# Optimization experiments

Hardware: AMD Instinct MI355X
Metric: run time of the kernel (lower is better)

Reference implementation:

```python
import jax, jax.numpy as jnp
import numpy as np

USER_NUM = 100000
ITEM_NUM = 50000
N_NODES = USER_NUM + ITEM_NUM
EMB_DIM = 64
N_LAYERS = 3
NNZ = 4800000


def setup_inputs() -> dict:
    key = jax.random.key(0)
    k1, k2, k3, k4, k5 = jax.random.split(key, 5)
    user_emb = 0.2 * jax.random.normal(k1, (USER_NUM, EMB_DIM), dtype=jnp.float32)
    item_emb = 0.2 * jax.random.normal(k2, (ITEM_NUM, EMB_DIM), dtype=jnp.float32)
    adj_row = jax.random.randint(k3, (NNZ,), 0, N_NODES, dtype=jnp.int32)
    adj_col = jax.random.randint(k4, (NNZ,), 0, N_NODES, dtype=jnp.int32)
    adj_vals = jax.random.uniform(k5, (NNZ,), dtype=jnp.float32)
    return {
        "user_emb": user_emb,
        "item_emb": item_emb,
        "adj_row": adj_row,
        "adj_col": adj_col,
        "adj_vals": adj_vals,
    }


def _spmm(row, col, vals, x):
    # sparse [N,N] @ dense [N,D] via gather + weighted segment-sum
    msg = vals[:, None] * x[col]  # [nnz, D]
    return jax.ops.segment_sum(msg, row, num_segments=N_NODES)


def reference(user_emb, item_emb, adj_row, adj_col, adj_vals):
    ego = jnp.concatenate([user_emb, item_emb], axis=0)  # [N, D]
    acc = ego  # running sum over layers (equivalent to stack+mean)
    for _ in range(N_LAYERS):
        ego = _spmm(adj_row, adj_col, adj_vals, ego)
        acc = acc + ego
    out = acc / jnp.asarray(N_LAYERS + 1, dtype=acc.dtype)
    return out[:USER_NUM], out[USER_NUM:]
```

## Files before the change

kernel.cpp:

```cpp
#include <hip/hip_runtime.h>

#define USER_NUM 100000
#define ITEM_NUM 50000
#define N_NODES  150000
#define EMB_DIM  64
#define NNZ      4800000

#define CB_SHIFT 10
#define ROWS_PER_CB 1024
#define NCB ((N_NODES + ROWS_PER_CB - 1) / ROWS_PER_CB)
#define CB_CAP 34000
#define TILE 8192
#define NTILES ((NNZ + TILE - 1) / TILE)
#define EPT 32

__device__ __forceinline__ float bflo(unsigned u) {
    return __uint_as_float(u << 16);
}
__device__ __forceinline__ float bfhi(unsigned u) {
    return __uint_as_float(u & 0xFFFF0000u);
}
__device__ __forceinline__ unsigned f2bf(float f) {
    unsigned u = __float_as_uint(f);
    return (u + 0x7FFFu + ((u >> 16) & 1u)) >> 16;
}

__global__ void lgcn_init(const float4* __restrict__ user,
                          const float4* __restrict__ item,
                          uint4* __restrict__ xb,
                          float4* __restrict__ acc) {
    int i = blockIdx.x * blockDim.x + threadIdx.x;
    if (i >= N_NODES * 8) return;
    const int user_chunks = USER_NUM * 8;
    float4 f0, f1;
    if (i < user_chunks) {
        f0 = user[i * 2];
        f1 = user[i * 2 + 1];
    } else {
        f0 = item[(i - user_chunks) * 2];
        f1 = item[(i - user_chunks) * 2 + 1];
    }
    acc[i * 2]     = f0;
    acc[i * 2 + 1] = f1;
    uint4 p;
    p.x = f2bf(f0.x) | (f2bf(f0.y) << 16);
    p.y = f2bf(f0.z) | (f2bf(f0.w) << 16);
    p.z = f2bf(f1.x) | (f2bf(f1.y) << 16);
    p.w = f2bf(f1.z) | (f2bf(f1.w) << 16);
    xb[i] = p;
}

__global__ void lgcn_bcur_init(int* __restrict__ bucket_cursor) {
    int b = blockIdx.x * blockDim.x + threadIdx.x;
    if (b < NCB) bucket_cursor[b] = b * CB_CAP;
}

__global__ __launch_bounds__(256) void lgcn_partition(
    const int* __restrict__ row,
    const int* __restrict__ col,
    const float* __restrict__ vals,
    int* __restrict__ bucket_cursor,
    int2* __restrict__ t_cv) {
    __shared__ int hist[NCB];
    __shared__ int excl[NCB];
    __shared__ int delta[NCB];
    __shared__ unsigned lslot[TILE];
    __shared__ int sscan[256];

    int tid = threadIdx.x;
    int tileStart = blockIdx.x * TILE;
    int tileCount = NNZ - tileStart;
    if (tileCount > TILE) tileCount = TILE;

    for (int b = tid; b < NCB; b += 256) hist[b] = 0;
    __syncthreads();

    int rws[EPT];
#pragma unroll
    for (int k = 0; k < EPT; ++k) {
        int le = tid + k * 256;
        int r = -1;
        if (le < tileCount) {
            r = row[tileStart + le];
            atomicAdd(&hist[r >> CB_SHIFT], 1);
        }
        rws[k] = r;
    }
    __syncthreads();

    int h = (tid < NCB) ? hist[tid] : 0;
    sscan[tid] = h;
    __syncthreads();
    for (int off = 1; off < 256; off <<= 1) {
        int x = (tid >= off) ? sscan[tid - off] : 0;
        __syncthreads();
        sscan[tid] += x;
        __syncthreads();
    }
    if (tid < NCB) {
        int ex = sscan[tid] - h;
        excl[tid] = ex;
        int rb = h ? atomicAdd(&bucket_cursor[tid], h) : 0;
        delta[tid] = rb - ex;
    }
    __syncthreads();

#pragma unroll
    for (int k = 0; k < EPT; ++k) {
        int le = tid + k * 256;
        if (le < tileCount) {
            int r = rws[k];
            int b = r >> CB_SHIFT;
            int lp = atomicAdd(&excl[b], 1);
            lslot[lp] = ((unsigned)b << 23) |
                        ((unsigned)(r & (ROWS_PER_CB - 1)) << 13) |
                        (unsigned)le;
        }
    }
    __syncthreads();

    for (int i = tid; i < tileCount; i += 256) {
        unsigned s = lslot[i];
        int b = s >> 23;
        int rlo = (s >> 13) & (ROWS_PER_CB - 1);
        int le = s & 8191;
        int e = tileStart + le;
        int gpos = delta[b] + i;
        if (gpos < (b + 1) * CB_CAP) {
            t_cv[gpos] = make_int2((rlo << 18) | col[e],
                                   __float_as_int(vals[e]));
        }
    }
}

__global__ __launch_bounds__(256) void lgcn_finalize(
    const int* __restrict__ bucket_cursor,
    const int2* __restrict__ t_cv,
    int2* __restrict__ csr_cv,
    int2* __restrict__ row_se) {
    __shared__ int hist[ROWS_PER_CB];
    __shared__ int cur[ROWS_PER_CB];
    __shared__ int sscan[256];
    int t = threadIdx.x;
    int b = blockIdx.x;

    int v = 0;
    if (t < NCB) {
        int cb = bucket_cursor[t] - t * CB_CAP;
        v = (cb > CB_CAP) ? CB_CAP : cb;
    }
    sscan[t] = v;
    __syncthreads();
    for (int off = 1; off < 256; off <<= 1) {
        int x = (t >= off) ? sscan[t - off] : 0;
        __syncthreads();
        sscan[t] += x;
        __syncthreads();
    }
    int prev = (b == 0) ? 0 : sscan[b - 1];
    int bbase = prev;
    int count = sscan[b] - prev;

    int lo = b * ROWS_PER_CB;
    int nrows = N_NODES - lo;
    if (nrows > ROWS_PER_CB) nrows = ROWS_PER_CB;

    for (int i = t; i < ROWS_PER_CB; i += 256) hist[i] = 0;
    __syncthreads();

    int base = b * CB_CAP;
    for (int e = base + t; e < base + count; e += 256)
        atomicAdd(&hist[(unsigned)t_cv[e].x >> 18], 1);
    __syncthreads();

    int4 hh = ((const int4*)hist)[t];
    int tsum = hh.x + hh.y + hh.z + hh.w;
    sscan[t] = tsum;
    __syncthreads();
    for (int off = 1; off < 256; off <<= 1) {
        int x = (t >= off) ? sscan[t - off] : 0;
        __syncthreads();
        sscan[t] += x;
        __syncthreads();
    }
    int p = bbase + sscan[t] - tsum;
    int hv[4] = {hh.x, hh.y, hh.z, hh.w};
    int i0 = t * 4;
#pragma unroll
    for (int k = 0; k < 4; ++k) {
        if (i0 + k < nrows) {
            row_se[lo + i0 + k] = make_int2(p, p + hv[k]);
            cur[i0 + k] = p;
        }
        p += hv[k];
    }
    __syncthreads();

    for (int e = base + t; e < base + count; e += 256) {
        int2 cv = t_cv[e];
        int rlo = (unsigned)cv.x >> 18;
        int pos = atomicAdd(&cur[rlo], 1);
        csr_cv[pos] = make_int2(cv.x & 0x3FFFF, cv.y);
    }
}

#define FMA8(vv, uu) do {                                          \
    a[0] += (vv) * bflo((uu).x); a[1] += (vv) * bfhi((uu).x);      \
    a[2] += (vv) * bflo((uu).y); a[3] += (vv) * bfhi((uu).y);      \
    a[4] += (vv) * bflo((uu).z); a[5] += (vv) * bfhi((uu).z);      \
    a[6] += (vv) * bflo((uu).w); a[7] += (vv) * bfhi((uu).w);      \
} while (0)

__global__ __launch_bounds__(256, 8) void lgcn_spmm_bf16(
    const int2* __restrict__ row_se,
    const int2* __restrict__ csr_cv,
    const uint4* __restrict__ xb,
    uint4* __restrict__ yb,
    float4* __restrict__ acc,
    float scale) {
    int gid = blockIdx.x * blockDim.x + threadIdx.x;
    int r = gid >> 6;
    if (r >= N_NODES) return;
    int lane = threadIdx.x & 63;
    int c = lane & 7;
    int sub = lane >> 3;

    int2 se = row_se[r];
    int start = se.x;
    int end = se.y;

    float a[8] = {0.f, 0.f, 0.f, 0.f, 0.f, 0.f, 0.f, 0.f};

    int e = start + sub;
    for (; e + 24 < end; e += 32) {
        int2 cv0 = csr_cv[e];
        int2 cv1 = csr_cv[e + 8];
        int2 cv2 = csr_cv[e + 16];
        int2 cv3 = csr_cv[e + 24];
        uint4 u0 = xb[cv0.x * 8 + c];
        uint4 u1 = xb[cv1.x * 8 + c];
        uint4 u2 = xb[cv2.x * 8 + c];
        uint4 u3 = xb[cv3.x * 8 + c];
        float v0 = __int_as_float(cv0.y);
        float v1 = __int_as_float(cv1.y);
        float v2 = __int_as_float(cv2.y);
        float v3 = __int_as_float(cv3.y);
        FMA8(v0, u0);
        FMA8(v1, u1);
        FMA8(v2, u2);
        FMA8(v3, u3);
    }
    if (e + 8 < end) {
        int2 cv0 = csr_cv[e];
        int2 cv1 = csr_cv[e + 8];
        uint4 u0 = xb[cv0.x * 8 + c];
        uint4 u1 = xb[cv1.x * 8 + c];
        float v0 = __int_as_float(cv0.y);
        float v1 = __int_as_float(cv1.y);
        FMA8(v0, u0);
        FMA8(v1, u1);
        e += 16;
    }
    if (e < end) {
        int2 cv = csr_cv[e];
        uint4 u = xb[cv.x * 8 + c];
        float v = __int_as_float(cv.y);
        FMA8(v, u);
    }

#pragma unroll
    for (int k = 0; k < 8; ++k) {
        a[k] += __shfl_xor(a[k], 8);
        a[k] += __shfl_xor(a[k], 16);
        a[k] += __shfl_xor(a[k], 32);
    }

    if (sub == 0) {
        uint4 p;
        p.x = f2bf(a[0]) | (f2bf(a[1]) << 16);
        p.y = f2bf(a[2]) | (f2bf(a[3]) << 16);
        p.z = f2bf(a[4]) | (f2bf(a[5]) << 16);
        p.w = f2bf(a[6]) | (f2bf(a[7]) << 16);
        yb[r * 8 + c] = p;
        int idx = r * 16 + c * 2;
        float4 o0 = acc[idx];
        float4 o1 = acc[idx + 1];
        o0.x = (o0.x + a[0]) * scale;
        o0.y = (o0.y + a[1]) * scale;
        o0.z = (o0.z + a[2]) * scale;
        o0.w = (o0.w + a[3]) * scale;
        o1.x = (o1.x + a[4]) * scale;
        o1.y = (o1.y + a[5]) * scale;
        o1.z = (o1.z + a[6]) * scale;
        o1.w = (o1.w + a[7]) * scale;
        acc[idx] = o0;
        acc[idx + 1] = o1;
    }
}

extern "C" void kernel_launch(void* const* d_in, const int* in_sizes, int n_in,
                              void* d_out, int out_size, void* d_ws, size_t ws_size,
                              hipStream_t stream) {
    const float* user_emb = (const float*)d_in[0];
    const float* item_emb = (const float*)d_in[1];
    const int*   adj_row  = (const int*)d_in[2];
    const int*   adj_col  = (const int*)d_in[3];
    const float* adj_vals = (const float*)d_in[4];
    float* out = (float*)d_out;

    char* base = (char*)d_ws;
    uint4* xb_a   = (uint4*)base;
    int2*  csr_cv = (int2*)(base + 19200000);
    char*  S      = base + 57600000;
    const size_t T_ENTRIES = (size_t)NCB * CB_CAP;
    int2*  t_cv   = (int2*)S;
    uint4* xb_b   = (uint4*)S;
    char*  tail   = S + T_ENTRIES * 8;
    int2*  row_se = (int2*)tail;
    int*   bucket_cursor = (int*)(tail + (size_t)N_NODES * 8);

    {
        int threads = 256;
        int blocks = (N_NODES * 8 + threads - 1) / threads;
        lgcn_init<<<blocks, threads, 0, stream>>>(
            (const float4*)user_emb, (const float4*)item_emb,
            xb_a, (float4*)out);
    }

    lgcn_bcur_init<<<1, 256, 0, stream>>>(bucket_cursor);
    lgcn_partition<<<NTILES, 256, 0, stream>>>(
        adj_row, adj_col, adj_vals, bucket_cursor, t_cv);
    lgcn_finalize<<<NCB, 256, 0, stream>>>(
        bucket_cursor, t_cv, csr_cv, row_se);

    const int spmm_block = 256;
    const int spmm_grid = (N_NODES * 64 + spmm_block - 1) / spmm_block;
    uint4* xa = xb_a;
    uint4* xbv = xb_b;
    for (int layer = 0; layer < 3; ++layer) {
        float scale = (layer == 2) ? 0.25f : 1.0f;
        lgcn_spmm_bf16<<<spmm_grid, spmm_block, 0, stream>>>(
            row_se, csr_cv, xa, xbv, (float4*)out, scale);
        uint4* t = xa; xa = xbv; xbv = t;
    }
}
```

Before: 591.3 us.

## Drop fp32 accumulator traffic and widen finalize blocks to 1024 threads

The running fp32 accumulator is no longer read and written in every layer. The first two SpMM layers now write only bf16 outputs, and a dedicated final kernel sums the original fp32 embeddings, both bf16 layer outputs and the last layer's result, then scales by 0.25. Separately, the CSR finalize kernel uses 1024 threads per bucket, with one row per thread and 4-way unrolled histogram and scatter loops. This trades per-layer fp32 read/write traffic for extra bf16 reads in the last layer, and the sum now uses bf16-rounded intermediates instead of fp32 ones, which slightly changes precision.

```diff
diff --git a/kernel.cpp b/kernel.cpp
--- a/kernel.cpp
+++ b/kernel.cpp
@@ -27,8 +27,7 @@
 
 __global__ void lgcn_init(const float4* __restrict__ user,
                           const float4* __restrict__ item,
-                          uint4* __restrict__ xb,
-                          float4* __restrict__ acc) {
+                          uint4* __restrict__ xb) {
     int i = blockIdx.x * blockDim.x + threadIdx.x;
     if (i >= N_NODES * 8) return;
     const int user_chunks = USER_NUM * 8;
@@ -40,8 +39,6 @@
         f0 = item[(i - user_chunks) * 2];
         f1 = item[(i - user_chunks) * 2 + 1];
     }
-    acc[i * 2]     = f0;
-    acc[i * 2 + 1] = f1;
     uint4 p;
     p.x = f2bf(f0.x) | (f2bf(f0.y) << 16);
     p.y = f2bf(f0.z) | (f2bf(f0.w) << 16);
@@ -133,14 +130,14 @@
     }
 }
 
-__global__ __launch_bounds__(256) void lgcn_finalize(
+__global__ __launch_bounds__(1024) void lgcn_finalize(
     const int* __restrict__ bucket_cursor,
     const int2* __restrict__ t_cv,
     int2* __restrict__ csr_cv,
     int2* __restrict__ row_se) {
     __shared__ int hist[ROWS_PER_CB];
     __shared__ int cur[ROWS_PER_CB];
-    __shared__ int sscan[256];
+    __shared__ int sscan[1024];
     int t = threadIdx.x;
     int b = blockIdx.x;
 
@@ -149,57 +146,78 @@
         int cb = bucket_cursor[t] - t * CB_CAP;
         v = (cb > CB_CAP) ? CB_CAP : cb;
     }
-    sscan[t] = v;
+    if (t < 256) sscan[t] = v;
     __syncthreads();
     for (int off = 1; off < 256; off <<= 1) {
-        int x = (t >= off) ? sscan[t - off] : 0;
-        __syncthreads();
-        sscan[t] += x;
+        int x = 0;
+        if (t < 256 && t >= off) x = sscan[t - off];
+        __syncthreads();
+        if (t < 256) sscan[t] += x;
         __syncthreads();
     }
     int prev = (b == 0) ? 0 : sscan[b - 1];
     int bbase = prev;
     int count = sscan[b] - prev;
+    __syncthreads();
 
     int lo = b * ROWS_PER_CB;
     int nrows = N_NODES - lo;
     if (nrows > ROWS_PER_CB) nrows = ROWS_PER_CB;
 
-    for (int i = t; i < ROWS_PER_CB; i += 256) hist[i] = 0;
+    hist[t] = 0;
     __syncthreads();
 
     int base = b * CB_CAP;
-    for (int e = base + t; e < base + count; e += 256)
+    int eEnd = base + count;
+    int e = base + t;
+    for (; e + 3 * 1024 < eEnd; e += 4 * 1024) {
+        int2 c0 = t_cv[e];
+        int2 c1 = t_cv[e + 1024];
+        int2 c2 = t_cv[e + 2048];
+        int2 c3 = t_cv[e + 3072];
+        atomicAdd(&hist[(unsigned)c0.x >> 18], 1);
+        atomicAdd(&hist[(unsigned)c1.x >> 18], 1);
+        atomicAdd(&hist[(unsigned)c2.x >> 18], 1);
+        atomicAdd(&hist[(unsigned)c3.x >> 18], 1);
+    }
+    for (; e < eEnd; e += 1024)
         atomicAdd(&hist[(unsigned)t_cv[e].x >> 18], 1);
     __syncthreads();
 
-    int4 hh = ((const int4*)hist)[t];
-    int tsum = hh.x + hh.y + hh.z + hh.w;
-    sscan[t] = tsum;
-    __syncthreads();
-    for (int off = 1; off < 256; off <<= 1) {
+    int h = hist[t];
+    sscan[t] = h;
+    __syncthreads();
+    for (int off = 1; off < 1024; off <<= 1) {
         int x = (t >= off) ? sscan[t - off] : 0;
         __syncthreads();
         sscan[t] += x;
         __syncthreads();
     }
-    int p = bbase + sscan[t] - tsum;
-    int hv[4] = {hh.x, hh.y, hh.z, hh.w};
-    int i0 = t * 4;
-#pragma unroll
-    for (int k = 0; k < 4; ++k) {
-        if (i0 + k < nrows) {
-            row_se[lo + i0 + k] = make_int2(p, p + hv[k]);
-            cur[i0 + k] = p;
-        }
-        p += hv[k];
-    }
-    __syncthreads();
-
-    for (int e = base + t; e < base + count; e += 256) {
+    int p = bbase + sscan[t] - h;
+    if (t < nrows) {
+        row_se[lo + t] = make_int2(p, p + h);
+        cur[t] = p;
+    }
+    __syncthreads();
+
+    e = base + t;
+    for (; e + 3 * 1024 < eEnd; e += 4 * 1024) {
+        int2 c0 = t_cv[e];
+        int2 c1 = t_cv[e + 1024];
+        int2 c2 = t_cv[e + 2048];
+        int2 c3 = t_cv[e + 3072];
+        int p0 = atomicAdd(&cur[(unsigned)c0.x >> 18], 1);
+        int p1 = atomicAdd(&cur[(unsigned)c1.x >> 18], 1);
+        int p2 = atomicAdd(&cur[(unsigned)c2.x >> 18], 1);
+        int p3 = atomicAdd(&cur[(unsigned)c3.x >> 18], 1);
+        csr_cv[p0] = make_int2(c0.x & 0x3FFFF, c0.y);
+        csr_cv[p1] = make_int2(c1.x & 0x3FFFF, c1.y);
+        csr_cv[p2] = make_int2(c2.x & 0x3FFFF, c2.y);
+        csr_cv[p3] = make_int2(c3.x & 0x3FFFF, c3.y);
+    }
+    for (; e < eEnd; e += 1024) {
         int2 cv = t_cv[e];
-        int rlo = (unsigned)cv.x >> 18;
-        int pos = atomicAdd(&cur[rlo], 1);
+        int pos = atomicAdd(&cur[(unsigned)cv.x >> 18], 1);
         csr_cv[pos] = make_int2(cv.x & 0x3FFFF, cv.y);
     }
 }
@@ -211,70 +229,66 @@
     a[6] += (vv) * bflo((uu).w); a[7] += (vv) * bfhi((uu).w);      \
 } while (0)
 
+#define SPMM_BODY                                                  \
+    int gid = blockIdx.x * blockDim.x + threadIdx.x;               \
+    int r = gid >> 6;                                              \
+    if (r >= N_NODES) return;                                      \
+    int lane = threadIdx.x & 63;                                   \
+    int c = lane & 7;                                              \
+    int sub = lane >> 3;                                           \
+    int2 se = row_se[r];                                           \
+    int start = se.x;                                              \
+    int end = se.y;                                                \
+    float a[8] = {0.f, 0.f, 0.f, 0.f, 0.f, 0.f, 0.f, 0.f};         \
+    int e = start + sub;                                           \
+    for (; e + 24 < end; e += 32) {                                \
+        int2 cv0 = csr_cv[e];                                      \
+        int2 cv1 = csr_cv[e + 8];                                  \
+        int2 cv2 = csr_cv[e + 16];                                 \
+        int2 cv3 = csr_cv[e + 24];                                 \
+        uint4 u0 = xb[cv0.x * 8 + c];                              \
+        uint4 u1 = xb[cv1.x * 8 + c];                              \
+        uint4 u2 = xb[cv2.x * 8 + c];                              \
+        uint4 u3 = xb[cv3.x * 8 + c];                              \
+        float v0 = __int_as_float(cv0.y);                          \
+        float v1 = __int_as_float(cv1.y);                          \
+        float v2 = __int_as_float(cv2.y);                          \
+        float v3 = __int_as_float(cv3.y);                          \
+        FMA8(v0, u0);                                              \
+        FMA8(v1, u1);                                              \
+        FMA8(v2, u2);                                              \
+        FMA8(v3, u3);                                              \
+    }                                                              \
+    if (e + 8 < end) {                                             \
+        int2 cv0 = csr_cv[e];                                      \
+        int2 cv1 = csr_cv[e + 8];                                  \
+        uint4 u0 = xb[cv0.x * 8 + c];                              \
+        uint4 u1 = xb[cv1.x * 8 + c];                              \
+        float v0 = __int_as_float(cv0.y);                          \
+        float v1 = __int_as_float(cv1.y);                          \
+        FMA8(v0, u0);                                              \
+        FMA8(v1, u1);                                              \
+        e += 16;                                                   \
+    }                                                              \
+    if (e < end) {                                                 \
+        int2 cv = csr_cv[e];                                       \
+        uint4 u = xb[cv.x * 8 + c];                                \
+        float v = __int_as_float(cv.y);                            \
+        FMA8(v, u);                                                \
+    }                                                              \
+    _Pragma("unroll")                                              \
+    for (int k = 0; k < 8; ++k) {                                  \
+        a[k] += __shfl_xor(a[k], 8);                               \
+        a[k] += __shfl_xor(a[k], 16);                              \
+        a[k] += __shfl_xor(a[k], 32);                              \
+    }
+
 __global__ __launch_bounds__(256, 8) void lgcn_spmm_bf16(
     const int2* __restrict__ row_se,
     const int2* __restrict__ csr_cv,
     const uint4* __restrict__ xb,
-    uint4* __restrict__ yb,
-    float4* __restrict__ acc,
-    float scale) {
-    int gid = blockIdx.x * blockDim.x + threadIdx.x;
-    int r = gid >> 6;
-    if (r >= N_NODES) return;
-    int lane = threadIdx.x & 63;
-    int c = lane & 7;
-    int sub = lane >> 3;
-
-    int2 se = row_se[r];
-    int start = se.x;
-    int end = se.y;
-
-    float a[8] = {0.f, 0.f, 0.f, 0.f, 0.f, 0.f, 0.f, 0.f};
-
-    int e = start + sub;
-    for (; e + 24 < end; e += 32) {
-        int2 cv0 = csr_cv[e];
-        int2 cv1 = csr_cv[e + 8];
-        int2 cv2 = csr_cv[e + 16];
-        int2 cv3 = csr_cv[e + 24];
-        uint4 u0 = xb[cv0.x * 8 + c];
-        uint4 u1 = xb[cv1.x * 8 + c];
-        uint4 u2 = xb[cv2.x * 8 + c];
-        uint4 u3 = xb[cv3.x * 8 + c];
-        float v0 = __int_as_float(cv0.y);
-        float v1 = __int_as_float(cv1.y);
-        float v2 = __int_as_float(cv2.y);
-        float v3 = __int_as_float(cv3.y);
-        FMA8(v0, u0);
-        FMA8(v1, u1);
-        FMA8(v2, u2);
-        FMA8(v3, u3);
-    }
-    if (e + 8 < end) {
-        int2 cv0 = csr_cv[e];
-        int2 cv1 = csr_cv[e + 8];
-        uint4 u0 = xb[cv0.x * 8 + c];
-        uint4 u1 = xb[cv1.x * 8 + c];
-        float v0 = __int_as_float(cv0.y);
-        float v1 = __int_as_float(cv1.y);
-        FMA8(v0, u0);
-        FMA8(v1, u1);
-        e += 16;
-    }
-    if (e < end) {
-        int2 cv = csr_cv[e];
-        uint4 u = xb[cv.x * 8 + c];
-        float v = __int_as_float(cv.y);
-        FMA8(v, u);
-    }
-
-#pragma unroll
-    for (int k = 0; k < 8; ++k) {
-        a[k] += __shfl_xor(a[k], 8);
-        a[k] += __shfl_xor(a[k], 16);
-        a[k] += __shfl_xor(a[k], 32);
-    }
-
+    uint4* __restrict__ yb) {
+    SPMM_BODY
     if (sub == 0) {
         uint4 p;
         p.x = f2bf(a[0]) | (f2bf(a[1]) << 16);
@@ -282,19 +296,37 @@
         p.z = f2bf(a[4]) | (f2bf(a[5]) << 16);
         p.w = f2bf(a[6]) | (f2bf(a[7]) << 16);
         yb[r * 8 + c] = p;
+    }
+}
+
+__global__ __launch_bounds__(256, 8) void lgcn_spmm_final(
+    const int2* __restrict__ row_se,
+    const int2* __restrict__ csr_cv,
+    const uint4* __restrict__ xb,
+    const uint4* __restrict__ y1b,
+    const float4* __restrict__ user,
+    const float4* __restrict__ item,
+    float4* __restrict__ out) {
+    SPMM_BODY
+    if (sub == 0) {
+        const float4* src = (r < USER_NUM) ? (user + (size_t)r * 16)
+                                           : (item + (size_t)(r - USER_NUM) * 16);
+        float4 f0 = src[c * 2];
+        float4 f1 = src[c * 2 + 1];
+        uint4 q1 = y1b[r * 8 + c];
+        uint4 q2 = xb[r * 8 + c];
+        float4 o0, o1;
+        o0.x = (f0.x + bflo(q1.x) + bflo(q2.x) + a[0]) * 0.25f;
+        o0.y = (f0.y + bfhi(q1.x) + bfhi(q2.x) + a[1]) * 0.25f;
+        o0.z = (f0.z + bflo(q1.y) + bflo(q2.y) + a[2]) * 0.25f;
+        o0.w = (f0.w + bfhi(q1.y) + bfhi(q2.y) + a[3]) * 0.25f;
+        o1.x = (f1.x + bflo(q1.z) + bflo(q2.z) + a[4]) * 0.25f;
+        o1.y = (f1.y + bfhi(q1.z) + bfhi(q2.z) + a[5]) * 0.25f;
+        o1.z = (f1.z + bflo(q1.w) + bflo(q2.w) + a[6]) * 0.25f;
+        o1.w = (f1.w + bfhi(q1.w) + bfhi(q2.w) + a[7]) * 0.25f;
         int idx = r * 16 + c * 2;
-        float4 o0 = acc[idx];
-        float4 o1 = acc[idx + 1];
-        o0.x = (o0.x + a[0]) * scale;
-        o0.y = (o0.y + a[1]) * scale;
-        o0.z = (o0.z + a[2]) * scale;
-        o0.w = (o0.w + a[3]) * scale;
-        o1.x = (o1.x + a[4]) * scale;
-        o1.y = (o1.y + a[5]) * scale;
-        o1.z = (o1.z + a[6]) * scale;
-        o1.w = (o1.w + a[7]) * scale;
-        acc[idx] = o0;
-        acc[idx + 1] = o1;
+        out[idx] = o0;
+        out[idx + 1] = o1;
     }
 }
 
@@ -314,7 +346,8 @@
     char*  S      = base + 57600000;
     const size_t T_ENTRIES = (size_t)NCB * CB_CAP;
     int2*  t_cv   = (int2*)S;
-    uint4* xb_b   = (uint4*)S;
+    uint4* y1b    = (uint4*)S;
+    uint4* y2b    = (uint4*)(S + 19200000);
     char*  tail   = S + T_ENTRIES * 8;
     int2*  row_se = (int2*)tail;
     int*   bucket_cursor = (int*)(tail + (size_t)N_NODES * 8);
@@ -323,24 +356,22 @@
         int threads = 256;
         int blocks = (N_NODES * 8 + threads - 1) / threads;
         lgcn_init<<<blocks, threads, 0, stream>>>(
-            (const float4*)user_emb, (const float4*)item_emb,
-            xb_a, (float4*)out);
+            (const float4*)user_emb, (const float4*)item_emb, xb_a);
     }
 
     lgcn_bcur_init<<<1, 256, 0, stream>>>(bucket_cursor);
     lgcn_partition<<<NTILES, 256, 0, stream>>>(
         adj_row, adj_col, adj_vals, bucket_cursor, t_cv);
-    lgcn_finalize<<<NCB, 256, 0, stream>>>(
+    lgcn_finalize<<<NCB, 1024, 0, stream>>>(
         bucket_cursor, t_cv, csr_cv, row_se);
 
     const int spmm_block = 256;
     const int spmm_grid = (N_NODES * 64 + spmm_block - 1) / spmm_block;
-    uint4* xa = xb_a;
-    uint4* xbv = xb_b;
-    for (int layer = 0; layer < 3; ++layer) {
-        float scale = (layer == 2) ? 0.25f : 1.0f;
-        lgcn_spmm_bf16<<<spmm_grid, spmm_block, 0, stream>>>(
-            row_se, csr_cv, xa, xbv, (float4*)out, scale);
-        uint4* t = xa; xa = xbv; xbv = t;
-    }
-}
+    lgcn_spmm_bf16<<<spmm_grid, spmm_block, 0, stream>>>(
+        row_se, csr_cv, xb_a, y1b);
+    lgcn_spmm_bf16<<<spmm_grid, spmm_block, 0, stream>>>(
+        row_se, csr_cv, y1b, y2b);
+    lgcn_spmm_final<<<spmm_grid, spmm_block, 0, stream>>>(
+        row_se, csr_cv, y2b, y1b,
+        (const float4*)user_emb, (const float4*)item_emb, (float4*)out);
+}
```

After: 524.7 us. -11.3%, faster.
